# Kernel optimization log

Hardware: AMD Instinct MI355X
Metric: run time of the kernel (lower is better)

The kernel has to match this reference:

```python
import jax, jax.numpy as jnp
import numpy as np

N = 100000   # nodes
E = 1600000  # edges
F = 256      # in/out feature dim
H = 64       # hidden dim


def _gcn_conv(x, edge_index, W, b):
    """PyG GCNConv: add self-loops, symmetric deg^-1/2 normalization, spmm, bias."""
    n = x.shape[0]
    loop = jnp.arange(n)
    src = jnp.concatenate([edge_index[0], loop])
    dst = jnp.concatenate([edge_index[1], loop])
    deg = jax.ops.segment_sum(jnp.ones(src.shape[0], dtype=x.dtype), dst, num_segments=n)
    dinv = jnp.where(deg > 0, deg ** -0.5, 0.0)
    norm = dinv[src] * dinv[dst]          # [E+N]
    h = x @ W                             # [N, out]
    out = jax.ops.segment_sum(h[src] * norm[:, None], dst, num_segments=n)
    return out + b


def _transformer_conv(x, edge_index, Wq, bq, Wk, bk, Wv, bv, Ws, bs):
    """PyG TransformerConv(heads=1): per-edge dot-product attention, softmax over
    incoming edges of each target node, weighted aggregate + root (skip) linear."""
    n = x.shape[0]
    src, dst = edge_index[0], edge_index[1]
    q = x @ Wq + bq
    k = x @ Wk + bk
    v = x @ Wv + bv
    scale = 1.0 / jnp.sqrt(jnp.asarray(q.shape[-1], x.dtype))
    logits = jnp.sum(q[dst] * k[src], axis=-1) * scale      # [E]
    m = jax.ops.segment_max(logits, dst, num_segments=n)
    m = jax.lax.stop_gradient(jnp.where(jnp.isfinite(m), m, 0.0))
    e = jnp.exp(logits - m[dst])                            # [E]
    denom = jax.ops.segment_sum(e, dst, num_segments=n)     # [N]
    agg = jax.ops.segment_sum(e[:, None] * v[src], dst, num_segments=n)  # [N, H]
    out = agg / jnp.where(denom > 0, denom, 1.0)[:, None]
    return out + x @ Ws + bs


def setup_inputs() -> dict:
    key = jax.random.key(0)
    ks = jax.random.split(key, 12)
    def lin(k, fan_in, fan_out):
        return jax.random.normal(k, (fan_in, fan_out), dtype=jnp.float32) / np.sqrt(fan_in)
    return {
        "x": jax.random.normal(ks[0], (N, F), dtype=jnp.float32),
        "edge_index": jax.random.randint(ks[1], (2, E), 0, N, dtype=jnp.int64),
        "W1": lin(ks[2], F, H), "b1": jnp.zeros((H,), jnp.float32),
        "Wq": lin(ks[3], H, H), "bq": jnp.zeros((H,), jnp.float32),
        "Wk": lin(ks[4], H, H), "bk": jnp.zeros((H,), jnp.float32),
        "Wv": lin(ks[5], H, H), "bv": jnp.zeros((H,), jnp.float32),
        "Ws": lin(ks[6], H, H), "bs": jnp.zeros((H,), jnp.float32),
        "W2": lin(ks[7], H, F), "b2": jnp.zeros((F,), jnp.float32),
    }


def reference(x, edge_index, W1, b1, Wq, bq, Wk, bk, Wv, bv, Ws, bs, W2, b2):
    h = _gcn_conv(x, edge_index, W1, b1)            # GCNConv(256 -> 64)
    h = jax.nn.relu(h)
    h = _transformer_conv(h, edge_index, Wq, bq, Wk, bk, Wv, bv, Ws, bs)  # TransformerConv(64->64)
    out = _gcn_conv(h, edge_index, W2, b2)          # GCNConv(64 -> 256)
    return out
```

## Files before the change

### kernel.cpp

```cpp
#include <hip/hip_runtime.h>
#include <hip/hip_bf16.h>

typedef unsigned short u16;
typedef unsigned int u32;

__device__ __forceinline__ float bl(u32 u) { union { u32 i; float f; } c; c.i = u << 16; return c.f; }
__device__ __forceinline__ float bh(u32 u) { union { u32 i; float f; } c; c.i = u & 0xffff0000u; return c.f; }
__device__ __forceinline__ u16 f2us(float f) {
    __hip_bfloat16 h = __float2bfloat16(f);
    return *reinterpret_cast<u16*>(&h);
}
__device__ __forceinline__ u32 pk2(float a, float b) {
    return (u32)f2us(a) | ((u32)f2us(b) << 16);
}
__device__ __forceinline__ void up8(uint4 u, float* f) {
    f[0] = bl(u.x); f[1] = bh(u.x); f[2] = bl(u.y); f[3] = bh(u.y);
    f[4] = bl(u.z); f[5] = bh(u.z); f[6] = bl(u.w); f[7] = bh(u.w);
}

typedef short bf16x8 __attribute__((ext_vector_type(8)));
typedef float f32x4 __attribute__((ext_vector_type(4)));

__global__ void k_hist(const int* __restrict__ dst, int* __restrict__ cnt, int E) {
    int e = blockIdx.x * 256 + threadIdx.x;
    if (e < E) atomicAdd(&cnt[dst[e]], 1);
}

__global__ void k_blocksum(const int* __restrict__ cnt, int* __restrict__ bsums, int n) {
    int base = blockIdx.x * 1024;
    int t = threadIdx.x;
    int s = 0;
    for (int j = t; j < 1024; j += 256) { int i = base + j; if (i < n) s += cnt[i]; }
    __shared__ int red[256];
    red[t] = s; __syncthreads();
    for (int off = 128; off > 0; off >>= 1) { if (t < off) red[t] += red[t + off]; __syncthreads(); }
    if (t == 0) bsums[blockIdx.x] = red[0];
}

__global__ void k_scan_bsums(int* __restrict__ bsums, int nb) {
    int t = threadIdx.x;
    int i0 = t * 4;
    int v[4]; int s = 0;
    #pragma unroll
    for (int j = 0; j < 4; j++) { v[j] = (i0 + j < nb) ? bsums[i0 + j] : 0; s += v[j]; }
    __shared__ int sc[256];
    sc[t] = s; __syncthreads();
    int acc = s;
    for (int off = 1; off < 256; off <<= 1) {
        int add = (t >= off) ? sc[t - off] : 0;
        __syncthreads();
        acc += add; sc[t] = acc;
        __syncthreads();
    }
    int run = acc - s;
    #pragma unroll
    for (int j = 0; j < 4; j++) {
        if (i0 + j < nb) { bsums[i0 + j] = run; run += v[j]; }
    }
}

__global__ void k_scan_final(int* __restrict__ cnt, const int* __restrict__ bsums,
                             int* __restrict__ rowptr, float* __restrict__ dinv, int n, int E) {
    int base = blockIdx.x * 1024;
    int t = threadIdx.x;
    int i0 = base + t * 4;
    int v[4]; int s = 0;
    for (int j = 0; j < 4; j++) { int i = i0 + j; v[j] = (i < n) ? cnt[i] : 0; s += v[j]; }
    __shared__ int sc[256];
    sc[t] = s; __syncthreads();
    int acc = s;
    for (int off = 1; off < 256; off <<= 1) {
        int add = (t >= off) ? sc[t - off] : 0;
        __syncthreads();
        acc += add; sc[t] = acc;
        __syncthreads();
    }
    int run = acc - s + bsums[blockIdx.x];
    for (int j = 0; j < 4; j++) {
        int i = i0 + j;
        if (i < n) {
            rowptr[i] = run;
            dinv[i] = rsqrtf((float)(v[j] + 1));
            cnt[i] = run;
            run += v[j];
        }
    }
    if (blockIdx.x == 0 && t == 0) rowptr[n] = E;
}

__global__ void k_scatter(const int* __restrict__ ei, int* __restrict__ cursor,
                          const float* __restrict__ dinv,
                          int2* __restrict__ edat, int E, int N) {
    int xcd = blockIdx.x & 7;
    int chunk = blockIdx.x >> 3;
    int nchunks = gridDim.x >> 3;
    int per = (E + nchunks - 1) / nchunks;
    int beg = chunk * per;
    int end = min(beg + per, E);
    int lo = (int)(((long long)N * xcd) >> 3);
    int hi = (int)(((long long)N * (xcd + 1)) >> 3);
    for (int e = beg + (int)threadIdx.x; e < end; e += 256) {
        int d = ei[E + e];
        if (d >= lo && d < hi) {
            int s = ei[e];
            int pos = atomicAdd(&cursor[d], 1);
            edat[pos] = make_int2(s, __float_as_int(dinv[s] * dinv[d]));
        }
    }
}

__global__ void k_wprep(const float* __restrict__ W1, const float* __restrict__ W2,
                        const float* __restrict__ Wq, const float* __restrict__ Wk,
                        const float* __restrict__ Wv, const float* __restrict__ Ws,
                        u16* __restrict__ W1t, u16* __restrict__ W2b, u16* __restrict__ Wcat) {
    int i = blockIdx.x * 256 + threadIdx.x;
    if (i < 16384) {
        W2b[i] = f2us(W2[i]);
    } else if (i < 32768) {
        int j = i - 16384; int col = j >> 8, k = j & 255;
        W1t[j] = f2us(W1[k * 64 + col]);
    } else if (i < 49152) {
        int j = i - 32768; int col = j >> 6, k = j & 63;
        int m = col >> 6, mc = col & 63;
        const float* src = (m == 0) ? Wq : (m == 1) ? Wk : (m == 2) ? Wv : Ws;
        Wcat[j] = f2us(src[k * 64 + mc]);
    }
}

__global__ __launch_bounds__(256) void k_gemm1(const float* __restrict__ x,
                                               const u16* __restrict__ W1t,
                                               u16* __restrict__ xw1b, int n) {
    __shared__ u16 xs[16][264];
    int t = threadIdx.x, w = t >> 6, l = t & 63;
    int base = blockIdx.x * 16;
    int row = t >> 4, seg = t & 15;
    int node = base + row;
    const float4* src = (const float4*)(x + (size_t)(node < n ? node : n - 1) * 256 + seg * 16);
    float4 f0 = src[0], f1 = src[1], f2 = src[2], f3 = src[3];
    uint4 o0, o1;
    o0.x = pk2(f0.x, f0.y); o0.y = pk2(f0.z, f0.w);
    o0.z = pk2(f1.x, f1.y); o0.w = pk2(f1.z, f1.w);
    o1.x = pk2(f2.x, f2.y); o1.y = pk2(f2.z, f2.w);
    o1.z = pk2(f3.x, f3.y); o1.w = pk2(f3.z, f3.w);
    u16* dst = &xs[row][seg * 16];
    *(uint4*)dst = o0; *(uint4*)(dst + 8) = o1;
    __syncthreads();
    int c = l & 15, kg = l >> 4;
    int col = w * 16 + c;
    f32x4 acc = {0.f, 0.f, 0.f, 0.f};
    #pragma unroll
    for (int kk = 0; kk < 8; kk++) {
        bf16x8 a = *(const bf16x8*)&xs[c][kk * 32 + kg * 8];
        bf16x8 b = *(const bf16x8*)&W1t[(size_t)col * 256 + kk * 32 + kg * 8];
        acc = __builtin_amdgcn_mfma_f32_16x16x32_bf16(a, b, acc, 0, 0, 0);
    }
    #pragma unroll
    for (int r = 0; r < 4; r++) {
        int nd = base + kg * 4 + r;
        if (nd < n) xw1b[(size_t)nd * 64 + col] = f2us(acc[r]);
    }
}

__global__ __launch_bounds__(256) void k_agg1(const u16* __restrict__ xw1b,
                                              const int2* __restrict__ edat,
                                              const int* __restrict__ rowptr,
                                              const float* __restrict__ dinv,
                                              const float* __restrict__ b1,
                                              float* __restrict__ B, int n) {
    int t = threadIdx.x;
    int w = t >> 6, l = t & 63, g = l >> 3, li = l & 7;
    int node = blockIdx.x * 4 + w;
    if (node >= n) return;
    int beg = rowptr[node], end = rowptr[node + 1];
    float a0[8], a1[8];
    #pragma unroll
    for (int j = 0; j < 8; j++) { a0[j] = 0.f; a1[j] = 0.f; }
    for (int e0 = beg; e0 < end; e0 += 16) {
        int eA = e0 + g, eB = e0 + 8 + g;
        bool vA = (eA < end), vB = (eB < end);
        int2 dA = vA ? edat[eA] : make_int2(0, 0);
        int2 dB = vB ? edat[eB] : make_int2(0, 0);
        uint4 uA = *(const uint4*)(xw1b + (size_t)dA.x * 64 + li * 8);
        uint4 uB = *(const uint4*)(xw1b + (size_t)dB.x * 64 + li * 8);
        float wA = __int_as_float(dA.y), wB = __int_as_float(dB.y);
        float fA[8]; up8(uA, fA);
        float fB[8]; up8(uB, fB);
        #pragma unroll
        for (int j = 0; j < 8; j++) { a0[j] += fA[j] * wA; a1[j] += fB[j] * wB; }
    }
    #pragma unroll
    for (int j = 0; j < 8; j++) a0[j] += a1[j];
    #pragma unroll
    for (int off = 8; off <= 32; off <<= 1)
        #pragma unroll
        for (int j = 0; j < 8; j++) a0[j] += __shfl_xor(a0[j], off);
    if (g == 0) {
        float di = dinv[node], di2 = di * di;
        uint4 u = *(const uint4*)(xw1b + (size_t)node * 64 + li * 8);
        float sf[8]; up8(u, sf);
        float4 bv0 = *(const float4*)(b1 + li * 8);
        float4 bv1 = *(const float4*)(b1 + li * 8 + 4);
        float bb[8] = {bv0.x, bv0.y, bv0.z, bv0.w, bv1.x, bv1.y, bv1.z, bv1.w};
        float r[8];
        #pragma unroll
        for (int j = 0; j < 8; j++) r[j] = fmaxf(a0[j] + sf[j] * di2 + bb[j], 0.f);
        float* dst = B + (size_t)node * 64 + li * 8;
        *(float4*)dst = make_float4(r[0], r[1], r[2], r[3]);
        *(float4*)(dst + 4) = make_float4(r[4], r[5], r[6], r[7]);
    }
}

__global__ __launch_bounds__(256) void k_lin_qkvs(float* __restrict__ B,
                                                  const u16* __restrict__ Wcat,
                                                  const float* __restrict__ bq, const float* __restrict__ bk,
                                                  const float* __restrict__ bv, const float* __restrict__ bs,
                                                  u16* __restrict__ kvb, u16* __restrict__ h2b, int n) {
    __shared__ u16 hs[16][72];
    int t = threadIdx.x, w = t >> 6, l = t & 63;
    int base = blockIdx.x * 16;
    int row = t >> 4, q4 = t & 15;
    int node = base + row;
    if (node < n) {
        float4 f = *(const float4*)(B + (size_t)node * 64 + q4 * 4);
        uint2 o; o.x = pk2(f.x, f.y); o.y = pk2(f.z, f.w);
        *(uint2*)&hs[row][q4 * 4] = o;
    }
    __syncthreads();
    int c = l & 15, kg = l >> 4;
    bf16x8 a0 = *(const bf16x8*)&hs[c][kg * 8];
    bf16x8 a1 = *(const bf16x8*)&hs[c][32 + kg * 8];
    #pragma unroll
    for (int ti = 0; ti < 4; ti++) {
        int col = (w * 4 + ti) * 16 + c;
        bf16x8 b0 = *(const bf16x8*)&Wcat[(size_t)col * 64 + kg * 8];
        bf16x8 b1 = *(const bf16x8*)&Wcat[(size_t)col * 64 + 32 + kg * 8];
        f32x4 acc = {0.f, 0.f, 0.f, 0.f};
        acc = __builtin_amdgcn_mfma_f32_16x16x32_bf16(a0, b0, acc, 0, 0, 0);
        acc = __builtin_amdgcn_mfma_f32_16x16x32_bf16(a1, b1, acc, 0, 0, 0);
        int m = col >> 6, mc = col & 63;
        float bias = ((m == 0) ? bq : (m == 1) ? bk : (m == 2) ? bv : bs)[mc];
        #pragma unroll
        for (int r = 0; r < 4; r++) {
            int nd = base + kg * 4 + r;
            if (nd < n) {
                float v = acc[r] + bias;
                if (m == 0)      B[(size_t)nd * 64 + mc] = v;
                else if (m == 1) kvb[(size_t)nd * 128 + mc] = f2us(v);
                else if (m == 2) kvb[(size_t)nd * 128 + 64 + mc] = f2us(v);
                else             h2b[(size_t)nd * 64 + mc] = f2us(v);
            }
        }
    }
}

__global__ __launch_bounds__(256) void k_attn(const float* __restrict__ B,
                                              const u16* __restrict__ kvb,
                                              const int2* __restrict__ edat,
                                              const int* __restrict__ rowptr,
                                              u16* __restrict__ h2b, int n) {
    int t = threadIdx.x;
    int w = t >> 6, l = t & 63, g = l >> 3, li = l & 7;
    int node = blockIdx.x * 4 + w;
    if (node >= n) return;
    const float* qp = B + (size_t)node * 64 + li * 8;
    float4 qa = *(const float4*)qp;
    float4 qb = *(const float4*)(qp + 4);
    float q[8] = {qa.x, qa.y, qa.z, qa.w, qb.x, qb.y, qb.z, qb.w};
    int beg = rowptr[node], end = rowptr[node + 1];
    float mA = -1e30f, denA = 0.f, mB = -1e30f, denB = 0.f;
    float accA[8], accB[8];
    #pragma unroll
    for (int j = 0; j < 8; j++) { accA[j] = 0.f; accB[j] = 0.f; }
    for (int e0 = beg; e0 < end; e0 += 16) {
        int eA = e0 + g, eB = e0 + 8 + g;
        bool vA = (eA < end), vB = (eB < end);
        int sA = vA ? edat[eA].x : 0;
        int sB = vB ? edat[eB].x : 0;
        const u16* rowA = kvb + (size_t)sA * 128;
        const u16* rowB = kvb + (size_t)sB * 128;
        uint4 kuA = *(const uint4*)(rowA + li * 8);
        uint4 vuA = *(const uint4*)(rowA + 64 + li * 8);
        uint4 kuB = *(const uint4*)(rowB + li * 8);
        uint4 vuB = *(const uint4*)(rowB + 64 + li * 8);
        float kf[8], vf[8];
        up8(kuA, kf); up8(vuA, vf);
        float dA = 0.f;
        #pragma unroll
        for (int j = 0; j < 8; j++) dA += q[j] * kf[j];
        dA += __shfl_xor(dA, 1);
        dA += __shfl_xor(dA, 2);
        dA += __shfl_xor(dA, 4);
        float logitA = vA ? dA * 0.125f : -1e30f;
        float nmA = fmaxf(mA, logitA);
        float rA = __expf(mA - nmA);
        float pA = vA ? __expf(logitA - nmA) : 0.f;
        denA = denA * rA + pA;
        #pragma unroll
        for (int j = 0; j < 8; j++) accA[j] = accA[j] * rA + pA * vf[j];
        mA = nmA;
        up8(kuB, kf); up8(vuB, vf);
        float dB = 0.f;
        #pragma unroll
        for (int j = 0; j < 8; j++) dB += q[j] * kf[j];
        dB += __shfl_xor(dB, 1);
        dB += __shfl_xor(dB, 2);
        dB += __shfl_xor(dB, 4);
        float logitB = vB ? dB * 0.125f : -1e30f;
        float nmB = fmaxf(mB, logitB);
        float rB = __expf(mB - nmB);
        float pB = vB ? __expf(logitB - nmB) : 0.f;
        denB = denB * rB + pB;
        #pragma unroll
        for (int j = 0; j < 8; j++) accB[j] = accB[j] * rB + pB * vf[j];
        mB = nmB;
    }
    float m = fmaxf(mA, mB);
    float rA = __expf(mA - m), rB = __expf(mB - m);
    float den = denA * rA + denB * rB;
    float acc[8];
    #pragma unroll
    for (int j = 0; j < 8; j++) acc[j] = accA[j] * rA + accB[j] * rB;
    #pragma unroll
    for (int off = 8; off <= 32; off <<= 1) {
        float mo = __shfl_xor(m, off);
        float deno = __shfl_xor(den, off);
        float nm = fmaxf(m, mo);
        float r = __expf(m - nm), ro = __expf(mo - nm);
        den = den * r + deno * ro;
        #pragma unroll
        for (int j = 0; j < 8; j++) {
            float ao = __shfl_xor(acc[j], off);
            acc[j] = acc[j] * r + ao * ro;
        }
        m = nm;
    }
    if (g == 0) {
        float inv = (den > 0.f) ? 1.f / den : 0.f;
        u16* hp = h2b + (size_t)node * 64 + li * 8;
        uint4 su = *(const uint4*)hp;
        float sk[8]; up8(su, sk);
        float o[8];
        #pragma unroll
        for (int j = 0; j < 8; j++) o[j] = acc[j] * inv + sk[j];
        uint4 ou;
        ou.x = pk2(o[0], o[1]); ou.y = pk2(o[2], o[3]);
        ou.z = pk2(o[4], o[5]); ou.w = pk2(o[6], o[7]);
        *(uint4*)hp = ou;
    }
}

__global__ __launch_bounds__(256) void k_agg2gemm2(const u16* __restrict__ h2b,
                                                   const int2* __restrict__ edat,
                                                   const int* __restrict__ rowptr,
                                                   const float* __restrict__ dinv,
                                                   const u16* __restrict__ W2b,
                                                   const float* __restrict__ b2,
                                                   float* __restrict__ out, int n) {
    __shared__ u16 ag[16][72];
    int t = threadIdx.x, w = t >> 6, l = t & 63, g = l >> 3, li = l & 7;
    int base = blockIdx.x * 16;
    for (int i = w; i < 16; i += 4) {
        int node = base + i;
        float a0[8], a1[8];
        #pragma unroll
        for (int j = 0; j < 8; j++) { a0[j] = 0.f; a1[j] = 0.f; }
        if (node < n) {
            int beg = rowptr[node], end = rowptr[node + 1];
            for (int e0 = beg; e0 < end; e0 += 16) {
                int eA = e0 + g, eB = e0 + 8 + g;
                bool vA = (eA < end), vB = (eB < end);
                int2 dA = vA ? edat[eA] : make_int2(0, 0);
                int2 dB = vB ? edat[eB] : make_int2(0, 0);
                uint4 uA = *(const uint4*)(h2b + (size_t)dA.x * 64 + li * 8);
                uint4 uB = *(const uint4*)(h2b + (size_t)dB.x * 64 + li * 8);
                float wA = __int_as_float(dA.y), wB = __int_as_float(dB.y);
                float fA[8]; up8(uA, fA);
                float fB[8]; up8(uB, fB);
                #pragma unroll
                for (int j = 0; j < 8; j++) { a0[j] += fA[j] * wA; a1[j] += fB[j] * wB; }
            }
        }
        #pragma unroll
        for (int j = 0; j < 8; j++) a0[j] += a1[j];
        #pragma unroll
        for (int off = 8; off <= 32; off <<= 1)
            #pragma unroll
            for (int j = 0; j < 8; j++) a0[j] += __shfl_xor(a0[j], off);
        if (g == 0) {
            if (node < n) {
                float di = dinv[node], di2 = di * di;
                uint4 u = *(const uint4*)(h2b + (size_t)node * 64 + li * 8);
                float sf[8]; up8(u, sf);
                #pragma unroll
                for (int j = 0; j < 8; j++) a0[j] += sf[j] * di2;
            }
            uint4 ou;
            ou.x = pk2(a0[0], a0[1]); ou.y = pk2(a0[2], a0[3]);
            ou.z = pk2(a0[4], a0[5]); ou.w = pk2(a0[6], a0[7]);
            *(uint4*)&ag[i][li * 8] = ou;
        }
    }
    __syncthreads();
    int c = l & 15;
    int kg = l >> 4;
    bf16x8 alo = *(const bf16x8*)&ag[c][kg * 8];
    bf16x8 ahi = *(const bf16x8*)&ag[c][32 + kg * 8];
    #pragma unroll
    for (int ti = 0; ti < 4; ti++) {
        int ct = w * 4 + ti;
        int col = ct * 16 + c;
        bf16x8 blo, bhi;
        #pragma unroll
        for (int j = 0; j < 8; j++) {
            blo[j] = (short)W2b[(kg * 8 + j) * 256 + col];
            bhi[j] = (short)W2b[(32 + kg * 8 + j) * 256 + col];
        }
        f32x4 acc = {0.f, 0.f, 0.f, 0.f};
        acc = __builtin_amdgcn_mfma_f32_16x16x32_bf16(alo, blo, acc, 0, 0, 0);
        acc = __builtin_amdgcn_mfma_f32_16x16x32_bf16(ahi, bhi, acc, 0, 0, 0);
        float bias = b2[col];
        #pragma unroll
        for (int r = 0; r < 4; r++) {
            int node = base + kg * 4 + r;
            if (node < n) out[(size_t)node * 256 + col] = acc[r] + bias;
        }
    }
}

extern "C" void kernel_launch(void* const* d_in, const int* in_sizes, int n_in,
                              void* d_out, int out_size, void* d_ws, size_t ws_size,
                              hipStream_t stream) {
    const float* x  = (const float*)d_in[0];
    const int*   ei = (const int*)d_in[1];
    const float* W1 = (const float*)d_in[2];
    const float* b1 = (const float*)d_in[3];
    const float* Wq = (const float*)d_in[4];
    const float* bq = (const float*)d_in[5];
    const float* Wk = (const float*)d_in[6];
    const float* bk = (const float*)d_in[7];
    const float* Wv = (const float*)d_in[8];
    const float* bv = (const float*)d_in[9];
    const float* Ws = (const float*)d_in[10];
    const float* bs = (const float*)d_in[11];
    const float* W2 = (const float*)d_in[12];
    const float* b2 = (const float*)d_in[13];
    float* out = (float*)d_out;

    const int N = in_sizes[0] / 256;
    const int E = in_sizes[1] / 2;

    char* ob = (char*)d_out;
    u16*   kvb  = (u16*)ob;
    u16*   xw1b = (u16*)(ob + (size_t)N * 128 * 2);
    float* B    = (float*)(ob + (size_t)N * 128 * 2 + (size_t)N * 64 * 2);

    char* p = (char*)d_ws;
    auto alloc = [&](size_t bytes) { char* r = p; p += (bytes + 255) & ~(size_t)255; return r; };
    int*   cnt    = (int*)alloc((size_t)N * 4);
    int*   rowptr = (int*)alloc((size_t)(N + 1) * 4);
    int*   bsums  = (int*)alloc(4096);
    int2*  edat   = (int2*)alloc((size_t)E * 8);
    float* dinv   = (float*)alloc((size_t)N * 4);
    u16*   h2b    = (u16*)alloc((size_t)N * 64 * 2);
    u16*   W2b    = (u16*)alloc((size_t)64 * 256 * 2);
    u16*   W1t    = (u16*)alloc((size_t)64 * 256 * 2);
    u16*   Wcat   = (u16*)alloc((size_t)256 * 64 * 2);

    const int NB = (N + 1023) / 1024;

    hipMemsetAsync(cnt, 0, (size_t)N * 4, stream);
    k_hist<<<(E + 255) / 256, 256, 0, stream>>>(ei + E, cnt, E);
    k_blocksum<<<NB, 256, 0, stream>>>(cnt, bsums, N);
    k_scan_bsums<<<1, 256, 0, stream>>>(bsums, NB);
    k_scan_final<<<NB, 256, 0, stream>>>(cnt, bsums, rowptr, dinv, N, E);
    k_scatter<<<512 * 8, 256, 0, stream>>>(ei, cnt, dinv, edat, E, N);
    k_wprep<<<192, 256, 0, stream>>>(W1, W2, Wq, Wk, Wv, Ws, W1t, W2b, Wcat);

    k_gemm1<<<(N + 15) / 16, 256, 0, stream>>>(x, W1t, xw1b, N);
    k_agg1<<<(N + 3) / 4, 256, 0, stream>>>(xw1b, edat, rowptr, dinv, b1, B, N);
    k_lin_qkvs<<<(N + 15) / 16, 256, 0, stream>>>(B, Wcat, bq, bk, bv, bs, kvb, h2b, N);
    k_attn<<<(N + 3) / 4, 256, 0, stream>>>(B, kvb, edat, rowptr, h2b, N);
    k_agg2gemm2<<<(N + 15) / 16, 256, 0, stream>>>(h2b, edat, rowptr, dinv, W2b, b2, out, N);
}
```

Measured before the change: 423.3 us.

## Build CSR via two-level bucket sort and fold normalization into node features

Replaces the single global-atomic scatter into an (src, weight) edge array with a two-pass bucketing scheme. Edges are first counted and placed into coarse per-bucket regions with per-block sub-counters, then each bucket is sorted into CSR slots using shared-memory atomics. The symmetric normalization is moved out of the edges: source features are pre-scaled by dinv and the destination scale is applied after aggregation, so edges store only a 4-byte source index. This cuts per-edge memory traffic in all three aggregation kernels and reduces global atomic contention, at the cost of extra kernel launches, an 8-byte-per-edge intermediate buffer, and extra passes over the edge list.

```diff
diff --git a/kernel.cpp b/kernel.cpp
--- a/kernel.cpp
+++ b/kernel.cpp
@@ -81,31 +81,72 @@
         if (i < n) {
             rowptr[i] = run;
             dinv[i] = rsqrtf((float)(v[j] + 1));
-            cnt[i] = run;
             run += v[j];
         }
     }
     if (blockIdx.x == 0 && t == 0) rowptr[n] = E;
 }
 
-__global__ void k_scatter(const int* __restrict__ ei, int* __restrict__ cursor,
-                          const float* __restrict__ dinv,
-                          int2* __restrict__ edat, int E, int N) {
-    int xcd = blockIdx.x & 7;
-    int chunk = blockIdx.x >> 3;
-    int nchunks = gridDim.x >> 3;
-    int per = (E + nchunks - 1) / nchunks;
-    int beg = chunk * per;
-    int end = min(beg + per, E);
-    int lo = (int)(((long long)N * xcd) >> 3);
-    int hi = (int)(((long long)N * (xcd + 1)) >> 3);
+__global__ void k_hist8(const int* __restrict__ ei, int E, int CH, int DPB,
+                        int* __restrict__ cnt8) {
+    int blk = blockIdx.x;
+    int beg = blk * CH, end = min(beg + CH, E);
+    int g = blk & 7;
     for (int e = beg + (int)threadIdx.x; e < end; e += 256) {
         int d = ei[E + e];
-        if (d >= lo && d < hi) {
-            int s = ei[e];
-            int pos = atomicAdd(&cursor[d], 1);
-            edat[pos] = make_int2(s, __float_as_int(dinv[s] * dinv[d]));
-        }
+        atomicAdd(&cnt8[(d / DPB) * 8 + g], 1);
+    }
+}
+
+__global__ void k_scan8(int* __restrict__ c, int n4) {
+    int t = threadIdx.x;
+    int i0 = t * 16;
+    int v[16]; int s = 0;
+    #pragma unroll
+    for (int j = 0; j < 16; j++) { v[j] = (i0 + j < n4) ? c[i0 + j] : 0; s += v[j]; }
+    __shared__ int sc[256];
+    sc[t] = s; __syncthreads();
+    int acc = s;
+    for (int off = 1; off < 256; off <<= 1) {
+        int add = (t >= off) ? sc[t - off] : 0;
+        __syncthreads();
+        acc += add; sc[t] = acc;
+        __syncthreads();
+    }
+    int run = acc - s;
+    #pragma unroll
+    for (int j = 0; j < 16; j++) {
+        if (i0 + j < n4) { c[i0 + j] = run; run += v[j]; }
+    }
+}
+
+__global__ void k_bucketA(const int* __restrict__ ei, int E, int CH, int DPB,
+                          int* __restrict__ cur8, int2* __restrict__ ebuf) {
+    int blk = blockIdx.x;
+    int beg = blk * CH, end = min(beg + CH, E);
+    int g = blk & 7;
+    for (int e = beg + (int)threadIdx.x; e < end; e += 256) {
+        int d = ei[E + e];
+        int s = ei[e];
+        int pos = atomicAdd(&cur8[(d / DPB) * 8 + g], 1);
+        ebuf[pos] = make_int2(s, d);
+    }
+}
+
+__global__ void k_bucketB(const int2* __restrict__ ebuf, const int* __restrict__ rowptr,
+                          int* __restrict__ csr, int N, int DPB) {
+    int b = blockIdx.x;
+    int lo = b * DPB;
+    if (lo >= N) return;
+    int hi = min(N, lo + DPB);
+    __shared__ int lcur[256];
+    for (int i = threadIdx.x; i < hi - lo; i += 256) lcur[i] = rowptr[lo + i];
+    __syncthreads();
+    int beg = rowptr[lo], end = rowptr[hi];
+    for (int e = beg + (int)threadIdx.x; e < end; e += 256) {
+        int2 r = ebuf[e];
+        int lp = atomicAdd(&lcur[r.y - lo], 1);
+        csr[lp] = r.x;
     }
 }
 
@@ -129,6 +170,7 @@
 
 __global__ __launch_bounds__(256) void k_gemm1(const float* __restrict__ x,
                                                const u16* __restrict__ W1t,
+                                               const float* __restrict__ dinv,
                                                u16* __restrict__ xw1b, int n) {
     __shared__ u16 xs[16][264];
     int t = threadIdx.x, w = t >> 6, l = t & 63;
@@ -157,12 +199,12 @@
     #pragma unroll
     for (int r = 0; r < 4; r++) {
         int nd = base + kg * 4 + r;
-        if (nd < n) xw1b[(size_t)nd * 64 + col] = f2us(acc[r]);
+        if (nd < n) xw1b[(size_t)nd * 64 + col] = f2us(acc[r] * dinv[nd]);
     }
 }
 
 __global__ __launch_bounds__(256) void k_agg1(const u16* __restrict__ xw1b,
-                                              const int2* __restrict__ edat,
+                                              const int* __restrict__ csr,
                                               const int* __restrict__ rowptr,
                                               const float* __restrict__ dinv,
                                               const float* __restrict__ b1,
@@ -178,11 +220,11 @@
     for (int e0 = beg; e0 < end; e0 += 16) {
         int eA = e0 + g, eB = e0 + 8 + g;
         bool vA = (eA < end), vB = (eB < end);
-        int2 dA = vA ? edat[eA] : make_int2(0, 0);
-        int2 dB = vB ? edat[eB] : make_int2(0, 0);
-        uint4 uA = *(const uint4*)(xw1b + (size_t)dA.x * 64 + li * 8);
-        uint4 uB = *(const uint4*)(xw1b + (size_t)dB.x * 64 + li * 8);
-        float wA = __int_as_float(dA.y), wB = __int_as_float(dB.y);
+        int sA = vA ? csr[eA] : 0;
+        int sB = vB ? csr[eB] : 0;
+        float wA = vA ? 1.f : 0.f, wB = vB ? 1.f : 0.f;
+        uint4 uA = *(const uint4*)(xw1b + (size_t)sA * 64 + li * 8);
+        uint4 uB = *(const uint4*)(xw1b + (size_t)sB * 64 + li * 8);
         float fA[8]; up8(uA, fA);
         float fB[8]; up8(uB, fB);
         #pragma unroll
@@ -195,7 +237,7 @@
         #pragma unroll
         for (int j = 0; j < 8; j++) a0[j] += __shfl_xor(a0[j], off);
     if (g == 0) {
-        float di = dinv[node], di2 = di * di;
+        float di = dinv[node];
         uint4 u = *(const uint4*)(xw1b + (size_t)node * 64 + li * 8);
         float sf[8]; up8(u, sf);
         float4 bv0 = *(const float4*)(b1 + li * 8);
@@ -203,7 +245,7 @@
         float bb[8] = {bv0.x, bv0.y, bv0.z, bv0.w, bv1.x, bv1.y, bv1.z, bv1.w};
         float r[8];
         #pragma unroll
-        for (int j = 0; j < 8; j++) r[j] = fmaxf(a0[j] + sf[j] * di2 + bb[j], 0.f);
+        for (int j = 0; j < 8; j++) r[j] = fmaxf((a0[j] + sf[j]) * di + bb[j], 0.f);
         float* dst = B + (size_t)node * 64 + li * 8;
         *(float4*)dst = make_float4(r[0], r[1], r[2], r[3]);
         *(float4*)(dst + 4) = make_float4(r[4], r[5], r[6], r[7]);
@@ -255,8 +297,9 @@
 
 __global__ __launch_bounds__(256) void k_attn(const float* __restrict__ B,
                                               const u16* __restrict__ kvb,
-                                              const int2* __restrict__ edat,
+                                              const int* __restrict__ csr,
                                               const int* __restrict__ rowptr,
+                                              const float* __restrict__ dinv,
                                               u16* __restrict__ h2b, int n) {
     int t = threadIdx.x;
     int w = t >> 6, l = t & 63, g = l >> 3, li = l & 7;
@@ -274,8 +317,8 @@
     for (int e0 = beg; e0 < end; e0 += 16) {
         int eA = e0 + g, eB = e0 + 8 + g;
         bool vA = (eA < end), vB = (eB < end);
-        int sA = vA ? edat[eA].x : 0;
-        int sB = vB ? edat[eB].x : 0;
+        int sA = vA ? csr[eA] : 0;
+        int sB = vB ? csr[eB] : 0;
         const u16* rowA = kvb + (size_t)sA * 128;
         const u16* rowB = kvb + (size_t)sB * 128;
         uint4 kuA = *(const uint4*)(rowA + li * 8);
@@ -336,12 +379,13 @@
     }
     if (g == 0) {
         float inv = (den > 0.f) ? 1.f / den : 0.f;
+        float di = dinv[node];
         u16* hp = h2b + (size_t)node * 64 + li * 8;
         uint4 su = *(const uint4*)hp;
         float sk[8]; up8(su, sk);
         float o[8];
         #pragma unroll
-        for (int j = 0; j < 8; j++) o[j] = acc[j] * inv + sk[j];
+        for (int j = 0; j < 8; j++) o[j] = (acc[j] * inv + sk[j]) * di;
         uint4 ou;
         ou.x = pk2(o[0], o[1]); ou.y = pk2(o[2], o[3]);
         ou.z = pk2(o[4], o[5]); ou.w = pk2(o[6], o[7]);
@@ -350,7 +394,7 @@
 }
 
 __global__ __launch_bounds__(256) void k_agg2gemm2(const u16* __restrict__ h2b,
-                                                   const int2* __restrict__ edat,
+                                                   const int* __restrict__ csr,
                                                    const int* __restrict__ rowptr,
                                                    const float* __restrict__ dinv,
                                                    const u16* __restrict__ W2b,
@@ -369,11 +413,11 @@
             for (int e0 = beg; e0 < end; e0 += 16) {
                 int eA = e0 + g, eB = e0 + 8 + g;
                 bool vA = (eA < end), vB = (eB < end);
-                int2 dA = vA ? edat[eA] : make_int2(0, 0);
-                int2 dB = vB ? edat[eB] : make_int2(0, 0);
-                uint4 uA = *(const uint4*)(h2b + (size_t)dA.x * 64 + li * 8);
-                uint4 uB = *(const uint4*)(h2b + (size_t)dB.x * 64 + li * 8);
-                float wA = __int_as_float(dA.y), wB = __int_as_float(dB.y);
+                int sA = vA ? csr[eA] : 0;
+                int sB = vB ? csr[eB] : 0;
+                float wA = vA ? 1.f : 0.f, wB = vB ? 1.f : 0.f;
+                uint4 uA = *(const uint4*)(h2b + (size_t)sA * 64 + li * 8);
+                uint4 uB = *(const uint4*)(h2b + (size_t)sB * 64 + li * 8);
                 float fA[8]; up8(uA, fA);
                 float fB[8]; up8(uB, fB);
                 #pragma unroll
@@ -388,11 +432,11 @@
             for (int j = 0; j < 8; j++) a0[j] += __shfl_xor(a0[j], off);
         if (g == 0) {
             if (node < n) {
-                float di = dinv[node], di2 = di * di;
+                float di = dinv[node];
                 uint4 u = *(const uint4*)(h2b + (size_t)node * 64 + li * 8);
                 float sf[8]; up8(u, sf);
                 #pragma unroll
-                for (int j = 0; j < 8; j++) a0[j] += sf[j] * di2;
+                for (int j = 0; j < 8; j++) a0[j] = (a0[j] + sf[j]) * di;
             }
             uint4 ou;
             ou.x = pk2(a0[0], a0[1]); ou.y = pk2(a0[2], a0[3]);
@@ -449,6 +493,11 @@
     const int N = in_sizes[0] / 256;
     const int E = in_sizes[1] / 2;
 
+    const int K = 512;
+    const int DPB = (N + K - 1) / K;
+    const int G = 2048;
+    const int CH = (E + G - 1) / G;
+
     char* ob = (char*)d_out;
     u16*   kvb  = (u16*)ob;
     u16*   xw1b = (u16*)(ob + (size_t)N * 128 * 2);
@@ -459,7 +508,9 @@
     int*   cnt    = (int*)alloc((size_t)N * 4);
     int*   rowptr = (int*)alloc((size_t)(N + 1) * 4);
     int*   bsums  = (int*)alloc(4096);
-    int2*  edat   = (int2*)alloc((size_t)E * 8);
+    int*   cnt8   = (int*)alloc((size_t)K * 8 * 4);
+    int*   csr    = (int*)alloc((size_t)E * 4);
+    int2*  ebuf   = (int2*)alloc((size_t)E * 8);
     float* dinv   = (float*)alloc((size_t)N * 4);
     u16*   h2b    = (u16*)alloc((size_t)N * 64 * 2);
     u16*   W2b    = (u16*)alloc((size_t)64 * 256 * 2);
@@ -469,16 +520,20 @@
     const int NB = (N + 1023) / 1024;
 
     hipMemsetAsync(cnt, 0, (size_t)N * 4, stream);
+    hipMemsetAsync(cnt8, 0, (size_t)K * 8 * 4, stream);
     k_hist<<<(E + 255) / 256, 256, 0, stream>>>(ei + E, cnt, E);
     k_blocksum<<<NB, 256, 0, stream>>>(cnt, bsums, N);
     k_scan_bsums<<<1, 256, 0, stream>>>(bsums, NB);
     k_scan_final<<<NB, 256, 0, stream>>>(cnt, bsums, rowptr, dinv, N, E);
-    k_scatter<<<512 * 8, 256, 0, stream>>>(ei, cnt, dinv, edat, E, N);
+    k_hist8<<<G, 256, 0, stream>>>(ei, E, CH, DPB, cnt8);
+    k_scan8<<<1, 256, 0, stream>>>(cnt8, K * 8);
+    k_bucketA<<<G, 256, 0, stream>>>(ei, E, CH, DPB, cnt8, ebuf);
+    k_bucketB<<<K, 256, 0, stream>>>(ebuf, rowptr, csr, N, DPB);
     k_wprep<<<192, 256, 0, stream>>>(W1, W2, Wq, Wk, Wv, Ws, W1t, W2b, Wcat);
 
-    k_gemm1<<<(N + 15) / 16, 256, 0, stream>>>(x, W1t, xw1b, N);
-    k_agg1<<<(N + 3) / 4, 256, 0, stream>>>(xw1b, edat, rowptr, dinv, b1, B, N);
+    k_gemm1<<<(N + 15) / 16, 256, 0, stream>>>(x, W1t, dinv, xw1b, N);
+    k_agg1<<<(N + 3) / 4, 256, 0, stream>>>(xw1b, csr, rowptr, dinv, b1, B, N);
     k_lin_qkvs<<<(N + 15) / 16, 256, 0, stream>>>(B, Wcat, bq, bk, bv, bs, kvb, h2b, N);
-    k_attn<<<(N + 3) / 4, 256, 0, stream>>>(B, kvb, edat, rowptr, h2b, N);
-    k_agg2gemm2<<<(N + 15) / 16, 256, 0, stream>>>(h2b, edat, rowptr, dinv, W2b, b2, out, N);
-}
+    k_attn<<<(N + 3) / 4, 256, 0, stream>>>(B, kvb, csr, rowptr, dinv, h2b, N);
+    k_agg2gemm2<<<(N + 15) / 16, 256, 0, stream>>>(h2b, csr, rowptr, dinv, W2b, b2, out, N);
+}
```

Result: slower. 598.2 us (+41.3%).

## Factor GCN normalization into node features and shrink CSR to source indices

Applied to the files above, without the earlier changes.

The symmetric GCN weight dinv[s]*dinv[d] is split so the source factor is applied once per node, in gemm1's output and in the attention output. The destination factor is applied after aggregation. This lets the CSR store only int source indices instead of int2 (source, weight) pairs, halving edge-array traffic in scatter, agg1, attn and agg2, and removes the dinv gather in scatter. Non-temporal loads are added for the edge streams. Scaling features before bf16 rounding shifts rounding slightly.

```diff
diff --git a/kernel.cpp b/kernel.cpp
--- a/kernel.cpp
+++ b/kernel.cpp
@@ -23,7 +23,7 @@
 
 __global__ void k_hist(const int* __restrict__ dst, int* __restrict__ cnt, int E) {
     int e = blockIdx.x * 256 + threadIdx.x;
-    if (e < E) atomicAdd(&cnt[dst[e]], 1);
+    if (e < E) atomicAdd(&cnt[__builtin_nontemporal_load(dst + e)], 1);
 }
 
 __global__ void k_blocksum(const int* __restrict__ cnt, int* __restrict__ bsums, int n) {
@@ -89,8 +89,7 @@
 }
 
 __global__ void k_scatter(const int* __restrict__ ei, int* __restrict__ cursor,
-                          const float* __restrict__ dinv,
-                          int2* __restrict__ edat, int E, int N) {
+                          int* __restrict__ csr, int E, int N) {
     int xcd = blockIdx.x & 7;
     int chunk = blockIdx.x >> 3;
     int nchunks = gridDim.x >> 3;
@@ -100,11 +99,11 @@
     int lo = (int)(((long long)N * xcd) >> 3);
     int hi = (int)(((long long)N * (xcd + 1)) >> 3);
     for (int e = beg + (int)threadIdx.x; e < end; e += 256) {
-        int d = ei[E + e];
+        int d = __builtin_nontemporal_load(ei + E + e);
         if (d >= lo && d < hi) {
-            int s = ei[e];
+            int s = __builtin_nontemporal_load(ei + e);
             int pos = atomicAdd(&cursor[d], 1);
-            edat[pos] = make_int2(s, __float_as_int(dinv[s] * dinv[d]));
+            csr[pos] = s;
         }
     }
 }
@@ -129,6 +128,7 @@
 
 __global__ __launch_bounds__(256) void k_gemm1(const float* __restrict__ x,
                                                const u16* __restrict__ W1t,
+                                               const float* __restrict__ dinv,
                                                u16* __restrict__ xw1b, int n) {
     __shared__ u16 xs[16][264];
     int t = threadIdx.x, w = t >> 6, l = t & 63;
@@ -157,12 +157,12 @@
     #pragma unroll
     for (int r = 0; r < 4; r++) {
         int nd = base + kg * 4 + r;
-        if (nd < n) xw1b[(size_t)nd * 64 + col] = f2us(acc[r]);
+        if (nd < n) xw1b[(size_t)nd * 64 + col] = f2us(acc[r] * dinv[nd]);
     }
 }
 
 __global__ __launch_bounds__(256) void k_agg1(const u16* __restrict__ xw1b,
-                                              const int2* __restrict__ edat,
+                                              const int* __restrict__ csr,
                                               const int* __restrict__ rowptr,
                                               const float* __restrict__ dinv,
                                               const float* __restrict__ b1,
@@ -178,11 +178,11 @@
     for (int e0 = beg; e0 < end; e0 += 16) {
         int eA = e0 + g, eB = e0 + 8 + g;
         bool vA = (eA < end), vB = (eB < end);
-        int2 dA = vA ? edat[eA] : make_int2(0, 0);
-        int2 dB = vB ? edat[eB] : make_int2(0, 0);
-        uint4 uA = *(const uint4*)(xw1b + (size_t)dA.x * 64 + li * 8);
-        uint4 uB = *(const uint4*)(xw1b + (size_t)dB.x * 64 + li * 8);
-        float wA = __int_as_float(dA.y), wB = __int_as_float(dB.y);
+        int sA = vA ? __builtin_nontemporal_load(csr + eA) : 0;
+        int sB = vB ? __builtin_nontemporal_load(csr + eB) : 0;
+        float wA = vA ? 1.f : 0.f, wB = vB ? 1.f : 0.f;
+        uint4 uA = *(const uint4*)(xw1b + (size_t)sA * 64 + li * 8);
+        uint4 uB = *(const uint4*)(xw1b + (size_t)sB * 64 + li * 8);
         float fA[8]; up8(uA, fA);
         float fB[8]; up8(uB, fB);
         #pragma unroll
@@ -195,7 +195,7 @@
         #pragma unroll
         for (int j = 0; j < 8; j++) a0[j] += __shfl_xor(a0[j], off);
     if (g == 0) {
-        float di = dinv[node], di2 = di * di;
+        float di = dinv[node];
         uint4 u = *(const uint4*)(xw1b + (size_t)node * 64 + li * 8);
         float sf[8]; up8(u, sf);
         float4 bv0 = *(const float4*)(b1 + li * 8);
@@ -203,7 +203,7 @@
         float bb[8] = {bv0.x, bv0.y, bv0.z, bv0.w, bv1.x, bv1.y, bv1.z, bv1.w};
         float r[8];
         #pragma unroll
-        for (int j = 0; j < 8; j++) r[j] = fmaxf(a0[j] + sf[j] * di2 + bb[j], 0.f);
+        for (int j = 0; j < 8; j++) r[j] = fmaxf((a0[j] + sf[j]) * di + bb[j], 0.f);
         float* dst = B + (size_t)node * 64 + li * 8;
         *(float4*)dst = make_float4(r[0], r[1], r[2], r[3]);
         *(float4*)(dst + 4) = make_float4(r[4], r[5], r[6], r[7]);
@@ -255,8 +255,9 @@
 
 __global__ __launch_bounds__(256) void k_attn(const float* __restrict__ B,
                                               const u16* __restrict__ kvb,
-                                              const int2* __restrict__ edat,
+                                              const int* __restrict__ csr,
                                               const int* __restrict__ rowptr,
+                                              const float* __restrict__ dinv,
                                               u16* __restrict__ h2b, int n) {
     int t = threadIdx.x;
     int w = t >> 6, l = t & 63, g = l >> 3, li = l & 7;
@@ -274,8 +275,8 @@
     for (int e0 = beg; e0 < end; e0 += 16) {
         int eA = e0 + g, eB = e0 + 8 + g;
         bool vA = (eA < end), vB = (eB < end);
-        int sA = vA ? edat[eA].x : 0;
-        int sB = vB ? edat[eB].x : 0;
+        int sA = vA ? __builtin_nontemporal_load(csr + eA) : 0;
+        int sB = vB ? __builtin_nontemporal_load(csr + eB) : 0;
         const u16* rowA = kvb + (size_t)sA * 128;
         const u16* rowB = kvb + (size_t)sB * 128;
         uint4 kuA = *(const uint4*)(rowA + li * 8);
@@ -336,12 +337,13 @@
     }
     if (g == 0) {
         float inv = (den > 0.f) ? 1.f / den : 0.f;
+        float di = dinv[node];
         u16* hp = h2b + (size_t)node * 64 + li * 8;
         uint4 su = *(const uint4*)hp;
         float sk[8]; up8(su, sk);
         float o[8];
         #pragma unroll
-        for (int j = 0; j < 8; j++) o[j] = acc[j] * inv + sk[j];
+        for (int j = 0; j < 8; j++) o[j] = (acc[j] * inv + sk[j]) * di;
         uint4 ou;
         ou.x = pk2(o[0], o[1]); ou.y = pk2(o[2], o[3]);
         ou.z = pk2(o[4], o[5]); ou.w = pk2(o[6], o[7]);
@@ -350,7 +352,7 @@
 }
 
 __global__ __launch_bounds__(256) void k_agg2gemm2(const u16* __restrict__ h2b,
-                                                   const int2* __restrict__ edat,
+                                                   const int* __restrict__ csr,
                                                    const int* __restrict__ rowptr,
                                                    const float* __restrict__ dinv,
                                                    const u16* __restrict__ W2b,
@@ -369,11 +371,11 @@
             for (int e0 = beg; e0 < end; e0 += 16) {
                 int eA = e0 + g, eB = e0 + 8 + g;
                 bool vA = (eA < end), vB = (eB < end);
-                int2 dA = vA ? edat[eA] : make_int2(0, 0);
-                int2 dB = vB ? edat[eB] : make_int2(0, 0);
-                uint4 uA = *(const uint4*)(h2b + (size_t)dA.x * 64 + li * 8);
-                uint4 uB = *(const uint4*)(h2b + (size_t)dB.x * 64 + li * 8);
-                float wA = __int_as_float(dA.y), wB = __int_as_float(dB.y);
+                int sA = vA ? __builtin_nontemporal_load(csr + eA) : 0;
+                int sB = vB ? __builtin_nontemporal_load(csr + eB) : 0;
+                float wA = vA ? 1.f : 0.f, wB = vB ? 1.f : 0.f;
+                uint4 uA = *(const uint4*)(h2b + (size_t)sA * 64 + li * 8);
+                uint4 uB = *(const uint4*)(h2b + (size_t)sB * 64 + li * 8);
                 float fA[8]; up8(uA, fA);
                 float fB[8]; up8(uB, fB);
                 #pragma unroll
@@ -388,11 +390,11 @@
             for (int j = 0; j < 8; j++) a0[j] += __shfl_xor(a0[j], off);
         if (g == 0) {
             if (node < n) {
-                float di = dinv[node], di2 = di * di;
+                float di = dinv[node];
                 uint4 u = *(const uint4*)(h2b + (size_t)node * 64 + li * 8);
                 float sf[8]; up8(u, sf);
                 #pragma unroll
-                for (int j = 0; j < 8; j++) a0[j] += sf[j] * di2;
+                for (int j = 0; j < 8; j++) a0[j] = (a0[j] + sf[j]) * di;
             }
             uint4 ou;
             ou.x = pk2(a0[0], a0[1]); ou.y = pk2(a0[2], a0[3]);
@@ -459,7 +461,7 @@
     int*   cnt    = (int*)alloc((size_t)N * 4);
     int*   rowptr = (int*)alloc((size_t)(N + 1) * 4);
     int*   bsums  = (int*)alloc(4096);
-    int2*  edat   = (int2*)alloc((size_t)E * 8);
+    int*   csr    = (int*)alloc((size_t)E * 4);
     float* dinv   = (float*)alloc((size_t)N * 4);
     u16*   h2b    = (u16*)alloc((size_t)N * 64 * 2);
     u16*   W2b    = (u16*)alloc((size_t)64 * 256 * 2);
@@ -473,12 +475,12 @@
     k_blocksum<<<NB, 256, 0, stream>>>(cnt, bsums, N);
     k_scan_bsums<<<1, 256, 0, stream>>>(bsums, NB);
     k_scan_final<<<NB, 256, 0, stream>>>(cnt, bsums, rowptr, dinv, N, E);
-    k_scatter<<<512 * 8, 256, 0, stream>>>(ei, cnt, dinv, edat, E, N);
+    k_scatter<<<512 * 8, 256, 0, stream>>>(ei, cnt, csr, E, N);
     k_wprep<<<192, 256, 0, stream>>>(W1, W2, Wq, Wk, Wv, Ws, W1t, W2b, Wcat);
 
-    k_gemm1<<<(N + 15) / 16, 256, 0, stream>>>(x, W1t, xw1b, N);
-    k_agg1<<<(N + 3) / 4, 256, 0, stream>>>(xw1b, edat, rowptr, dinv, b1, B, N);
+    k_gemm1<<<(N + 15) / 16, 256, 0, stream>>>(x, W1t, dinv, xw1b, N);
+    k_agg1<<<(N + 3) / 4, 256, 0, stream>>>(xw1b, csr, rowptr, dinv, b1, B, N);
     k_lin_qkvs<<<(N + 15) / 16, 256, 0, stream>>>(B, Wcat, bq, bk, bv, bs, kvb, h2b, N);
-    k_attn<<<(N + 3) / 4, 256, 0, stream>>>(B, kvb, edat, rowptr, h2b, N);
-    k_agg2gemm2<<<(N + 15) / 16, 256, 0, stream>>>(h2b, edat, rowptr, dinv, W2b, b2, out, N);
-}
+    k_attn<<<(N + 3) / 4, 256, 0, stream>>>(B, kvb, csr, rowptr, dinv, h2b, N);
+    k_agg2gemm2<<<(N + 15) / 16, 256, 0, stream>>>(h2b, csr, rowptr, dinv, W2b, b2, out, N);
+}
```

New measurement: 448.4 us. 5.9% more time.
